# Performance work log

Measured on AMD Instinct MI355X. Metric: run time of the kernel, lower is better.

The kernel has to match this reference:

```python
import jax, jax.numpy as jnp
import numpy as np

N, D, R = 65536, 32, 128


def setup_inputs() -> dict:
    key = jax.random.key(0)
    k1, k2, k3, k4 = jax.random.split(key, 4)
    X = jax.random.normal(k1, (N, D), dtype=jnp.float32)
    a = jax.random.normal(k2, (R, D), dtype=jnp.float32)
    b = jax.random.uniform(k3, (R, D), dtype=jnp.float32)  # positive, like abs(randn)
    c = jax.random.normal(k4, (R, D + 1), dtype=jnp.float32)
    return {"X": X, "a": a, "b": b, "c": c}


def reference(X, a, b, c):
    # Gaussian membership per (sample, rule, dim): exp(-(x-a)^2 / (2*clamp(b,1e-8)^2))
    b_cl = jnp.clip(b, 1e-8)                      # [R, D]
    diff = X[:, None, :] - a[None, :, :]          # [N, R, D]
    mu = jnp.exp(-(diff * diff) / (2.0 * b_cl * b_cl))
    strengths = jnp.prod(mu, axis=2)              # [N, R] rule firing strengths
    strengths_sum = jnp.sum(strengths, axis=1, keepdims=True)
    normalized = strengths / (strengths_sum + 1e-8)
    # consequent: linear model per rule, X @ c[:, :-1].T + bias
    rule_out = X @ c[:, :-1].T + c[:, -1]         # [N, R]
    predictions = jnp.sum(normalized * rule_out, axis=1)  # [N]
    return (predictions, strengths, normalized)
```

## Files before the change

### kernel.cpp

```cpp
#include <hip/hip_runtime.h>

#define NS 65536
#define DD 32
#define RR 128
#define SPB 16
#define STR 132

typedef float f2 __attribute__((ext_vector_type(2)));

static __device__ __forceinline__ f2 pkfma(f2 a, f2 b, f2 c) {
    f2 d;
    asm("v_pk_fma_f32 %0, %1, %2, %3" : "=v"(d) : "v"(a), "v"(b), "v"(c));
    return d;
}

__global__ __launch_bounds__(128, 3) void anfis_main(
    const float* __restrict__ X, const float* __restrict__ A,
    const float* __restrict__ B, const float* __restrict__ C,
    float* __restrict__ out_pred, float* __restrict__ out_str,
    float* __restrict__ out_norm)
{
    __shared__ float SBUF[SPB * STR];
    __shared__ float PBUF[SPB * STR];
    __shared__ float XT[SPB * DD];
    __shared__ float pS[SPB][8];
    __shared__ float pD[SPB][8];
    __shared__ float scale_lds[SPB];

    const int tid   = threadIdx.x;
    const int nbase = blockIdx.x * SPB;

    ((float4*)XT)[tid] = ((const float4*)(X + (size_t)nbase * DD))[tid];

    f2 w01_[8], w23_[8], n01_[8], n23_[8], c01_[8], c23_[8];
    float bias;
    {
        const float4* av = (const float4*)(A + tid * DD);
        const float4* bv = (const float4*)(B + tid * DD);
        #pragma unroll
        for (int i = 0; i < 8; ++i) {
            float4 va = av[i], vb = bv[i];
            float w0 = 0.8493218003f * __builtin_amdgcn_rcpf(fmaxf(vb.x, 1e-8f));
            float w1 = 0.8493218003f * __builtin_amdgcn_rcpf(fmaxf(vb.y, 1e-8f));
            float w2 = 0.8493218003f * __builtin_amdgcn_rcpf(fmaxf(vb.z, 1e-8f));
            float w3 = 0.8493218003f * __builtin_amdgcn_rcpf(fmaxf(vb.w, 1e-8f));
            w01_[i] = f2{w0, w1};            w23_[i] = f2{w2, w3};
            n01_[i] = f2{-va.x * w0, -va.y * w1};
            n23_[i] = f2{-va.z * w2, -va.w * w3};
            c01_[i] = f2{C[tid * (DD + 1) + 4*i + 0], C[tid * (DD + 1) + 4*i + 1]};
            c23_[i] = f2{C[tid * (DD + 1) + 4*i + 2], C[tid * (DD + 1) + 4*i + 3]};
        }
        bias = C[tid * (DD + 1) + DD];
    }
    __syncthreads();

    #pragma unroll
    for (int i = 0; i < 8; ++i)
        asm("" : "+v"(w01_[i]), "+v"(w23_[i]), "+v"(n01_[i]),
                 "+v"(n23_[i]), "+v"(c01_[i]), "+v"(c23_[i]));
    asm("" : "+v"(bias));

    #define LOADH(buf, jj, hh) { _Pragma("unroll") \
        for (int g = 0; g < 4; ++g) \
            buf[g] = *(const float4*)&XT[(jj) * DD + (hh) * 16 + g * 4]; }

    #define COMPUTEH(buf, gbase) { _Pragma("unroll") \
        for (int g = 0; g < 4; ++g) { \
            const int gi = (gbase) + g; \
            const f2* xp2 = (const f2*)&buf[g]; \
            f2 x01 = xp2[0], x23 = xp2[1]; \
            f2 t01 = pkfma(x01, w01_[gi], n01_[gi]); \
            s01 = pkfma(t01, t01, s01); \
            r01 = pkfma(x01, c01_[gi], r01); \
            f2 t23 = pkfma(x23, w23_[gi], n23_[gi]); \
            s23 = pkfma(t23, t23, s23); \
            r23 = pkfma(x23, c23_[gi], r23); \
        } }

    float4 qa[4], qb[4];
    LOADH(qa, 0, 0)
    #pragma unroll 2
    for (int j = 0; j < SPB; ++j) {
        f2 s01 = f2{0.f, 0.f}, s23 = f2{0.f, 0.f};
        f2 r01 = f2{bias, 0.f}, r23 = f2{0.f, 0.f};
        LOADH(qb, j, 1)
        COMPUTEH(qa, 0)
        LOADH(qa, (j + 1) & (SPB - 1), 0)
        COMPUTEH(qb, 4)
        float st = __builtin_amdgcn_exp2f(-((s01.x + s01.y) + (s23.x + s23.y)));
        float ro = (r01.x + r01.y) + (r23.x + r23.y);
        SBUF[j * STR + tid] = st;
        PBUF[j * STR + tid] = st * ro;
    }
    #undef LOADH
    #undef COMPUTEH
    __syncthreads();

    {
        int s = tid >> 3, o = tid & 7;
        const float4* srow = (const float4*)&SBUF[s * STR + o * 16];
        const float4* prow = (const float4*)&PBUF[s * STR + o * 16];
        float ss = 0.f, dd = 0.f;
        #pragma unroll
        for (int k = 0; k < 4; ++k) {
            float4 v = srow[k]; ss += (v.x + v.y) + (v.z + v.w);
            float4 p = prow[k]; dd += (p.x + p.y) + (p.z + p.w);
        }
        pS[s][o] = ss; pD[s][o] = dd;
    }
    __syncthreads();
    float predv = 0.f;
    if (tid < SPB) {
        float ss = 0.f, dd = 0.f;
        #pragma unroll
        for (int o = 0; o < 8; ++o) { ss += pS[tid][o]; dd += pD[tid][o]; }
        float sc = 1.0f / (ss + 1e-8f);
        predv = dd * sc;
        scale_lds[tid] = sc;
    }
    __syncthreads();
    if (tid < SPB) out_pred[nbase + tid] = predv;

    #pragma unroll
    for (int it = 0; it < 4; ++it) {
        int f   = it * 128 + tid;
        int row = f >> 5;
        int col = f & 31;
        float4 v = *(const float4*)&SBUF[row * STR + col * 4];
        float sc = scale_lds[row];
        size_t base = ((size_t)(nbase + row)) * RR + col * 4;
        *(float4*)(out_str  + base) = v;
        *(float4*)(out_norm + base) = make_float4(v.x * sc, v.y * sc, v.z * sc, v.w * sc);
    }
}

extern "C" void kernel_launch(void* const* d_in, const int* in_sizes, int n_in,
                              void* d_out, int out_size, void* d_ws, size_t ws_size,
                              hipStream_t stream) {
    const float* X = (const float*)d_in[0];
    const float* A = (const float*)d_in[1];
    const float* B = (const float*)d_in[2];
    const float* C = (const float*)d_in[3];

    float* pred = (float*)d_out;
    float* str  = pred + NS;
    float* nrm  = str + (size_t)NS * RR;

    anfis_main<<<dim3(NS / SPB), dim3(128), 0, stream>>>(X, A, B, C, pred, str, nrm);
}
```

Baseline: 105.2 us.

## Split each rule's dimensions across two lanes and double samples per block

Each rule is now handled by a pair of adjacent lanes, each covering 16 of the 32 input dimensions. The two partial sums are combined with a DPP lane swap, and one lane writes the strength while the other writes the weighted product. The block grows to 256 threads and 32 samples, which halves per-thread register state and should allow more waves in flight to hide latency. In exchange, the exp and the cross-lane reductions are computed twice per rule-sample pair, and the manual software pipelining of the sample loop is reshaped.

Result: faster. 100.3 us (-4.6%).

```diff
diff --git a/kernel.cpp b/kernel.cpp
--- a/kernel.cpp
+++ b/kernel.cpp
@@ -3,8 +3,9 @@
 #define NS 65536
 #define DD 32
 #define RR 128
-#define SPB 16
+#define SPB 32
 #define STR 132
+#define NBLK (NS / SPB)
 
 typedef float f2 __attribute__((ext_vector_type(2)));
 
@@ -14,7 +15,12 @@
     return d;
 }
 
-__global__ __launch_bounds__(128, 3) void anfis_main(
+static __device__ __forceinline__ float dpp_x1(float x) {
+    return __int_as_float(__builtin_amdgcn_update_dpp(
+        0, __float_as_int(x), 0xB1 , 0xF, 0xF, true));
+}
+
+__global__ __launch_bounds__(256, 4) void anfis_main(
     const float* __restrict__ X, const float* __restrict__ A,
     const float* __restrict__ B, const float* __restrict__ C,
     float* __restrict__ out_pred, float* __restrict__ out_str,
@@ -28,17 +34,21 @@
     __shared__ float scale_lds[SPB];
 
     const int tid   = threadIdx.x;
+    const int rule  = tid >> 1;
+    const int half  = tid & 1;
+    const int xoff  = half * 16;
     const int nbase = blockIdx.x * SPB;
 
     ((float4*)XT)[tid] = ((const float4*)(X + (size_t)nbase * DD))[tid];
 
-    f2 w01_[8], w23_[8], n01_[8], n23_[8], c01_[8], c23_[8];
-    float bias;
+    f2 w01_[4], w23_[4], n01_[4], n23_[4], c01_[4], c23_[4];
+    float biasv;
     {
-        const float4* av = (const float4*)(A + tid * DD);
-        const float4* bv = (const float4*)(B + tid * DD);
+        const float4* av = (const float4*)(A + rule * DD + xoff);
+        const float4* bv = (const float4*)(B + rule * DD + xoff);
+        const float*  cp = C + rule * (DD + 1) + xoff;
         #pragma unroll
-        for (int i = 0; i < 8; ++i) {
+        for (int i = 0; i < 4; ++i) {
             float4 va = av[i], vb = bv[i];
             float w0 = 0.8493218003f * __builtin_amdgcn_rcpf(fmaxf(vb.x, 1e-8f));
             float w1 = 0.8493218003f * __builtin_amdgcn_rcpf(fmaxf(vb.y, 1e-8f));
@@ -47,53 +57,56 @@
             w01_[i] = f2{w0, w1};            w23_[i] = f2{w2, w3};
             n01_[i] = f2{-va.x * w0, -va.y * w1};
             n23_[i] = f2{-va.z * w2, -va.w * w3};
-            c01_[i] = f2{C[tid * (DD + 1) + 4*i + 0], C[tid * (DD + 1) + 4*i + 1]};
-            c23_[i] = f2{C[tid * (DD + 1) + 4*i + 2], C[tid * (DD + 1) + 4*i + 3]};
+            c01_[i] = f2{cp[4*i + 0], cp[4*i + 1]};
+            c23_[i] = f2{cp[4*i + 2], cp[4*i + 3]};
         }
-        bias = C[tid * (DD + 1) + DD];
+        biasv = half ? C[rule * (DD + 1) + DD] : 0.0f;
     }
     __syncthreads();
 
     #pragma unroll
-    for (int i = 0; i < 8; ++i)
+    for (int i = 0; i < 4; ++i)
         asm("" : "+v"(w01_[i]), "+v"(w23_[i]), "+v"(n01_[i]),
                  "+v"(n23_[i]), "+v"(c01_[i]), "+v"(c23_[i]));
-    asm("" : "+v"(bias));
+    asm("" : "+v"(biasv));
 
-    #define LOADH(buf, jj, hh) { _Pragma("unroll") \
+    float* wbuf = half ? PBUF : SBUF;
+
+    #define LOADQ(buf, jj) { _Pragma("unroll") \
         for (int g = 0; g < 4; ++g) \
-            buf[g] = *(const float4*)&XT[(jj) * DD + (hh) * 16 + g * 4]; }
+            buf[g] = *(const float4*)&XT[(jj) * DD + xoff + g * 4]; }
 
-    #define COMPUTEH(buf, gbase) { _Pragma("unroll") \
+    #define DOSAMPLE(buf, jj) { \
+        f2 s01 = f2{0.f, 0.f}, s23 = f2{0.f, 0.f}; \
+        f2 r01 = f2{biasv, 0.f}, r23 = f2{0.f, 0.f}; \
+        _Pragma("unroll") \
         for (int g = 0; g < 4; ++g) { \
-            const int gi = (gbase) + g; \
             const f2* xp2 = (const f2*)&buf[g]; \
             f2 x01 = xp2[0], x23 = xp2[1]; \
-            f2 t01 = pkfma(x01, w01_[gi], n01_[gi]); \
+            f2 t01 = pkfma(x01, w01_[g], n01_[g]); \
             s01 = pkfma(t01, t01, s01); \
-            r01 = pkfma(x01, c01_[gi], r01); \
-            f2 t23 = pkfma(x23, w23_[gi], n23_[gi]); \
+            r01 = pkfma(x01, c01_[g], r01); \
+            f2 t23 = pkfma(x23, w23_[g], n23_[g]); \
             s23 = pkfma(t23, t23, s23); \
-            r23 = pkfma(x23, c23_[gi], r23); \
-        } }
+            r23 = pkfma(x23, c23_[g], r23); \
+        } \
+        float sh = (s01.x + s01.y) + (s23.x + s23.y); \
+        float rh = (r01.x + r01.y) + (r23.x + r23.y); \
+        float stot = sh + dpp_x1(sh); \
+        float rtot = rh + dpp_x1(rh); \
+        float st = __builtin_amdgcn_exp2f(-stot); \
+        wbuf[(jj) * STR + rule] = half ? st * rtot : st; }
 
     float4 qa[4], qb[4];
-    LOADH(qa, 0, 0)
-    #pragma unroll 2
-    for (int j = 0; j < SPB; ++j) {
-        f2 s01 = f2{0.f, 0.f}, s23 = f2{0.f, 0.f};
-        f2 r01 = f2{bias, 0.f}, r23 = f2{0.f, 0.f};
-        LOADH(qb, j, 1)
-        COMPUTEH(qa, 0)
-        LOADH(qa, (j + 1) & (SPB - 1), 0)
-        COMPUTEH(qb, 4)
-        float st = __builtin_amdgcn_exp2f(-((s01.x + s01.y) + (s23.x + s23.y)));
-        float ro = (r01.x + r01.y) + (r23.x + r23.y);
-        SBUF[j * STR + tid] = st;
-        PBUF[j * STR + tid] = st * ro;
+    LOADQ(qa, 0)
+    for (int j = 0; j < SPB; j += 2) {
+        LOADQ(qb, j + 1)
+        DOSAMPLE(qa, j)
+        if (j + 2 < SPB) LOADQ(qa, j + 2)
+        DOSAMPLE(qb, j + 1)
     }
-    #undef LOADH
-    #undef COMPUTEH
+    #undef LOADQ
+    #undef DOSAMPLE
     __syncthreads();
 
     {
@@ -123,7 +136,7 @@
 
     #pragma unroll
     for (int it = 0; it < 4; ++it) {
-        int f   = it * 128 + tid;
+        int f   = it * 256 + tid;
         int row = f >> 5;
         int col = f & 31;
         float4 v = *(const float4*)&SBUF[row * STR + col * 4];
@@ -146,5 +159,5 @@
     float* str  = pred + NS;
     float* nrm  = str + (size_t)NS * RR;
 
-    anfis_main<<<dim3(NS / SPB), dim3(128), 0, stream>>>(X, A, B, C, pred, str, nrm);
+    anfis_main<<<dim3(NBLK), dim3(256), 0, stream>>>(X, A, B, C, pred, str, nrm);
 }
```
